# Kernel optimization log

Measured on AMD Instinct MI355X. Metric: run time of the kernel, lower is better.

Reference implementation:

```python
import jax, jax.numpy as jnp
import numpy as np

N_NODES = 50000
N_EDGES = 800000
IN_DIM = 256
OUT_DIM = 64
NEG_SLOPE = 0.01  # torch F.leaky_relu default


def setup_inputs() -> dict:
    key = jax.random.key(0)
    k1, k2, k3, k4, k5 = jax.random.split(key, 5)
    h = jax.random.normal(k1, (N_NODES, IN_DIM), dtype=jnp.float32)
    W = jax.random.normal(k2, (OUT_DIM, IN_DIM), dtype=jnp.float32) * 0.05
    a = jax.random.normal(k3, (1, 2 * OUT_DIM), dtype=jnp.float32) * 0.05
    src = jax.random.randint(k4, (N_EDGES,), 0, N_NODES)
    dst = jax.random.randint(k5, (N_EDGES,), 0, N_NODES)
    return {"h": h, "W": W, "a": a, "src": src, "dst": dst}


def reference(h, W, a, src, dst):
    # node projection: z = fc(h)               [N, D_out]
    z = jnp.einsum("ni,oi->no", h, W)
    # edge attention: e = leaky_relu(attn_fc(concat(z_src, z_dst)))
    # split a into left/right halves to avoid materializing the [E, 2D] concat
    a_l, a_r = a[0, :OUT_DIM], a[0, OUT_DIM:]
    el = z @ a_l  # [N]
    er = z @ a_r  # [N]
    e = jax.nn.leaky_relu(el[src] + er[dst], negative_slope=NEG_SLOPE)  # [E]
    # segment softmax over incoming edges of each destination node
    m = jax.ops.segment_max(e, dst, num_segments=N_NODES)  # [N], -inf for isolated
    ex = jnp.exp(e - m[dst])                               # [E]
    s = jax.ops.segment_sum(ex, dst, num_segments=N_NODES)  # [N]
    alpha = ex / s[dst]                                     # [E]
    # weighted-sum aggregation of source features
    h_out = jax.ops.segment_sum(alpha[:, None] * z[src], dst, num_segments=N_NODES)
    return h_out
```

## Files before the change

kernel.cpp:

```cpp
#include <hip/hip_runtime.h>

#define IN_DIM 256
#define OUT_DIM 64
#define NEG_SLOPE 0.01f
#define CHUNK 4096

typedef __attribute__((ext_vector_type(8))) short short8v;
typedef __attribute__((ext_vector_type(4))) float float4v;

__device__ __forceinline__ unsigned short f2bf(float f) {
    unsigned u = __float_as_uint(f);
    return (unsigned short)((u + 0x7FFFu + ((u >> 16) & 1u)) >> 16);
}
__device__ __forceinline__ float bf2f(unsigned short u) {
    return __uint_as_float((unsigned)u << 16);
}

__global__ void k_init(const float* __restrict__ W, unsigned short* __restrict__ Wb,
                       int* __restrict__ bc, int* __restrict__ cursor) {
    int i = blockIdx.x * blockDim.x + threadIdx.x;
    if (i < OUT_DIM * IN_DIM) Wb[i] = f2bf(W[i]);
    if (i < 256) { bc[i] = 0; cursor[i] = 0; }
}

__global__ __launch_bounds__(256, 3) void k1_mfma_count(
        const float* __restrict__ h, const unsigned short* __restrict__ Wb,
        const float* __restrict__ a, const int* __restrict__ dst,
        unsigned short* __restrict__ zb, float* __restrict__ el, float* __restrict__ er,
        int* __restrict__ bc, int M, int E) {
    __shared__ uint4 wlds[2048];
    __shared__ int hist[256];
    hist[threadIdx.x] = 0;

    #pragma unroll
    for (int k = 0; k < 8; ++k) {
        int c = threadIdx.x + k * 256;
        int row = c >> 5, col = c & 31;
        wlds[(row << 5) | (col ^ (row & 7))] = ((const uint4*)Wb)[c];
    }
    __syncthreads();

    const int lane = threadIdx.x & 63;
    const int wid  = (blockIdx.x * 256 + threadIdx.x) >> 6;
    const int r0 = wid * 16;

    if (r0 < M) {
        const int lrow = lane & 15;
        const int kgrp = lane >> 4;
        const int k0   = kgrp * 8;
        const int swz  = lrow & 7;

        const float* __restrict__ hrow = h + (size_t)(r0 + lrow) * IN_DIM;

        float4 hreg[16];
        #pragma unroll
        for (int s = 0; s < 8; ++s) {
            hreg[2 * s]     = *(const float4*)(hrow + s * 32 + k0);
            hreg[2 * s + 1] = *(const float4*)(hrow + s * 32 + k0 + 4);
        }

        float4v acc[4];
        #pragma unroll
        for (int n = 0; n < 4; ++n) acc[n] = (float4v){0.f, 0.f, 0.f, 0.f};

        #pragma unroll
        for (int s = 0; s < 8; ++s) {
            float4 ha = hreg[2 * s], hb = hreg[2 * s + 1];
            short8v afrag;
            afrag[0] = (short)f2bf(ha.x); afrag[1] = (short)f2bf(ha.y);
            afrag[2] = (short)f2bf(ha.z); afrag[3] = (short)f2bf(ha.w);
            afrag[4] = (short)f2bf(hb.x); afrag[5] = (short)f2bf(hb.y);
            afrag[6] = (short)f2bf(hb.z); afrag[7] = (short)f2bf(hb.w);
            #pragma unroll
            for (int n = 0; n < 4; ++n) {
                const int slot = ((n * 16 + lrow) << 5) | ((s * 4 + kgrp) ^ swz);
                short8v bfrag = *(const short8v*)&wlds[slot];
                acc[n] = __builtin_amdgcn_mfma_f32_16x16x32_bf16(afrag, bfrag, acc[n], 0, 0, 0);
            }
        }

        float al4[4], ar4[4];
        #pragma unroll
        for (int n = 0; n < 4; ++n) {
            al4[n] = a[n * 16 + lrow];
            ar4[n] = a[OUT_DIM + n * 16 + lrow];
        }
        #pragma unroll
        for (int j = 0; j < 4; ++j) {
            const int row = r0 + kgrp * 4 + j;
            float vl = 0.f, vr = 0.f;
            #pragma unroll
            for (int n = 0; n < 4; ++n) {
                float v = acc[n][j];
                zb[(size_t)row * OUT_DIM + n * 16 + lrow] = f2bf(v);
                vl += v * al4[n];
                vr += v * ar4[n];
            }
            #pragma unroll
            for (int m = 8; m >= 1; m >>= 1) {
                vl += __shfl_xor(vl, m, 64);
                vr += __shfl_xor(vr, m, 64);
            }
            if (lrow == 0) { el[row] = vl; er[row] = vr; }
        }
    }

    __syncthreads();
    const int stride = gridDim.x * 256;
    for (int i = blockIdx.x * 256 + threadIdx.x; i < E; i += stride)
        atomicAdd(&hist[dst[i] >> 8], 1);
    __syncthreads();
    if (hist[threadIdx.x]) atomicAdd(&bc[threadIdx.x], hist[threadIdx.x]);
}

__global__ __launch_bounds__(256) void kA_scatter(
        const int* __restrict__ src, const int* __restrict__ dst,
        const int* __restrict__ bc, int* __restrict__ cursor,
        unsigned* __restrict__ bucketbuf, int E, int nbuck) {
    __shared__ unsigned stag[CHUNK];
    __shared__ int bsc[256], cnt[256], lofs[256], lcur[256], tb[256];
    const int t = threadIdx.x;
    const int base = blockIdx.x * CHUNK;
    const int n = min(CHUNK, E - base);

    int bv = (t < nbuck) ? bc[t] : 0;
    bsc[t] = bv;
    cnt[t] = 0;
    __syncthreads();
    for (int off = 1; off < 256; off <<= 1) {
        int add = (t >= off) ? bsc[t - off] : 0;
        __syncthreads();
        bsc[t] += add;
        __syncthreads();
    }
    const int bstart_t = bsc[t] - bv;

    int es[16], ed[16];
    #pragma unroll
    for (int k = 0; k < 16; ++k) {
        int p = t + k * 256;
        if (p < n) {
            es[k] = src[base + p];
            ed[k] = dst[base + p];
            atomicAdd(&cnt[ed[k] >> 8], 1);
        }
    }
    __syncthreads();

    lofs[t] = cnt[t];
    __syncthreads();
    for (int off = 1; off < 256; off <<= 1) {
        int add = (t >= off) ? lofs[t - off] : 0;
        __syncthreads();
        lofs[t] += add;
        __syncthreads();
    }
    lofs[t] -= cnt[t];
    __syncthreads();

    {
        int c = cnt[t];
        int g = c ? atomicAdd(&cursor[t], c) : 0;
        tb[t] = bstart_t + g - lofs[t];
    }
    lcur[t] = lofs[t];
    __syncthreads();

    #pragma unroll
    for (int k = 0; k < 16; ++k) {
        int p = t + k * 256;
        if (p < n) {
            int b = ed[k] >> 8;
            int pos = atomicAdd(&lcur[b], 1);
            stag[pos] = ((unsigned)ed[k] << 16) | (unsigned)es[k];
        }
    }
    __syncthreads();

    #pragma unroll
    for (int k = 0; k < 16; ++k) {
        int p = t + k * 256;
        if (p < n) {
            unsigned v = stag[p];
            int b = v >> 24;
            bucketbuf[tb[b] + p] = v;
        }
    }
}

__global__ __launch_bounds__(256) void kB_build(
        const unsigned* __restrict__ bucketbuf, const int* __restrict__ bc,
        int* __restrict__ csr_src, int* __restrict__ ends, int N, int nbuck) {
    __shared__ int sc[256], lcnt[256], lofs[256], lcur[256];
    __shared__ int s_start;
    const int b = blockIdx.x, t = threadIdx.x;

    int bv = (t < nbuck) ? bc[t] : 0;
    sc[t] = bv;
    lcnt[t] = 0;
    __syncthreads();
    for (int off = 1; off < 256; off <<= 1) {
        int add = (t >= off) ? sc[t - off] : 0;
        __syncthreads();
        sc[t] += add;
        __syncthreads();
    }
    if (t == b) s_start = sc[t] - bv;
    __syncthreads();

    const int start = s_start;
    const int cnt = bc[b];
    const int node0 = b << 8;
    const int nloc = min(256, N - node0);

    for (int i = t; i < cnt; i += 256)
        atomicAdd(&lcnt[(bucketbuf[start + i] >> 16) & 255], 1);
    __syncthreads();

    lofs[t] = lcnt[t];
    __syncthreads();
    for (int off = 1; off < 256; off <<= 1) {
        int add = (t >= off) ? lofs[t - off] : 0;
        __syncthreads();
        lofs[t] += add;
        __syncthreads();
    }
    if (t < nloc) ends[node0 + t] = start + lofs[t];
    lcur[t] = lofs[t] - lcnt[t];
    __syncthreads();

    for (int i = t; i < cnt; i += 256) {
        unsigned v = bucketbuf[start + i];
        int node = (v >> 16) & 255;
        int pos = atomicAdd(&lcur[node], 1);
        csr_src[start + pos] = (int)(v & 0xFFFFu);
    }
}

__global__ __launch_bounds__(256) void k5_node(
        const int* __restrict__ csr_src, const int* __restrict__ ends,
        const float* __restrict__ el, const float* __restrict__ er,
        const unsigned short* __restrict__ zb, float* __restrict__ out, int N) {
    const int lane = threadIdx.x & 63;
    const int node = blockIdx.x * 4 + (threadIdx.x >> 6);
    if (node >= N) return;

    const int start = (node == 0) ? 0 : ends[node - 1];
    const int end   = ends[node];
    const int deg   = end - start;
    float acc = 0.0f;

    if (deg > 0 && deg <= 64) {
        const float er_i = er[node];
        int   s0 = 0;
        float m  = -3.4e38f;
        float e0 = 0.0f;
        if (lane < deg) {
            s0 = csr_src[start + lane];
            float x = el[s0] + er_i;
            e0 = fmaxf(x, NEG_SLOPE * x);
            m  = e0;
        }
        #pragma unroll
        for (int msk = 32; msk; msk >>= 1) m = fmaxf(m, __shfl_xor(m, msk, 64));
        float ex0 = (lane < deg) ? __expf(e0 - m) : 0.0f;
        float sum = ex0;
        #pragma unroll
        for (int msk = 32; msk; msk >>= 1) sum += __shfl_xor(sum, msk, 64);
        const float inv = 1.0f / sum;

        float aq[8];
        #pragma unroll
        for (int q = 0; q < 8; ++q) aq[q] = 0.f;
        int r = 0;
        for (; r + 8 <= deg; r += 8) {
            int ss[8]; float ww[8];
            #pragma unroll
            for (int q = 0; q < 8; ++q) {
                ss[q] = __shfl(s0,  r + q, 64);
                ww[q] = __shfl(ex0, r + q, 64);
            }
            #pragma unroll
            for (int q = 0; q < 8; ++q)
                aq[q] += ww[q] * bf2f(zb[(size_t)ss[q] * OUT_DIM + lane]);
        }
        for (; r < deg; ++r) {
            int   sa = __shfl(s0,  r, 64);
            float wa = __shfl(ex0, r, 64);
            aq[0] += wa * bf2f(zb[(size_t)sa * OUT_DIM + lane]);
        }
        acc = (((aq[0] + aq[1]) + (aq[2] + aq[3])) +
               ((aq[4] + aq[5]) + (aq[6] + aq[7]))) * inv;
    } else if (deg > 64) {
        const float er_i = er[node];
        float e0 = 0.0f, e1 = 0.0f;
        int   s0 = 0,    s1 = 0;
        float m = -3.4e38f;
        int t = 0;
        for (int j = start + lane; j < end; j += 64, ++t) {
            int s = csr_src[j];
            float x = el[s] + er_i;
            float e = fmaxf(x, NEG_SLOPE * x);
            if (t == 0) { e0 = e; s0 = s; }
            else if (t == 1) { e1 = e; s1 = s; }
            m = fmaxf(m, e);
        }
        #pragma unroll
        for (int msk = 32; msk; msk >>= 1) m = fmaxf(m, __shfl_xor(m, msk, 64));
        float sum = 0.0f;
        t = 0;
        for (int j = start + lane; j < end; j += 64, ++t) {
            float e;
            if (t == 0) e = e0;
            else if (t == 1) e = e1;
            else {
                int s = csr_src[j];
                float x = el[s] + er_i;
                e = fmaxf(x, NEG_SLOPE * x);
            }
            float ex = __expf(e - m);
            if (t == 0) e0 = ex; else if (t == 1) e1 = ex;
            sum += ex;
        }
        #pragma unroll
        for (int msk = 32; msk; msk >>= 1) sum += __shfl_xor(sum, msk, 64);
        const float inv = 1.0f / sum;

        for (int r = 0; r < deg; ++r) {
            int tt = r >> 6, owner = r & 63;
            int s; float ex;
            if (tt == 0)      { s = __shfl(s0, owner, 64); ex = __shfl(e0, owner, 64); }
            else if (tt == 1) { s = __shfl(s1, owner, 64); ex = __shfl(e1, owner, 64); }
            else {
                s = csr_src[start + r];
                float x = el[s] + er_i;
                float e = fmaxf(x, NEG_SLOPE * x);
                ex = __expf(e - m);
            }
            acc += ex * bf2f(zb[(size_t)s * OUT_DIM + lane]);
        }
        acc *= inv;
    }
    out[(size_t)node * OUT_DIM + lane] = acc;
}

extern "C" void kernel_launch(void* const* d_in, const int* in_sizes, int n_in,
                              void* d_out, int out_size, void* d_ws, size_t ws_size,
                              hipStream_t stream) {
    const float* h   = (const float*)d_in[0];
    const float* W   = (const float*)d_in[1];
    const float* a   = (const float*)d_in[2];
    const int*   src = (const int*)d_in[3];
    const int*   dst = (const int*)d_in[4];
    float* out = (float*)d_out;

    const int N = in_sizes[0] / IN_DIM;
    const int E = in_sizes[3];
    const int nbuck = (N + 255) >> 8;

    unsigned short* zb = (unsigned short*)d_ws;
    float* el   = (float*)(zb + (size_t)N * OUT_DIM);
    float* er   = el + N;
    int*   ends = (int*)(er + N);
    int*   csr_src = ends + N;
    unsigned* bucketbuf = (unsigned*)(csr_src + E);
    int*   bc     = (int*)(bucketbuf + E);
    int*   cursor = bc + 256;
    unsigned short* Wb = (unsigned short*)(cursor + 256);

    k_init<<<(OUT_DIM * IN_DIM + 255) / 256, 256, 0, stream>>>(W, Wb, bc, cursor);
    {
        const int waves = (N + 15) / 16;
        k1_mfma_count<<<(waves + 3) / 4, 256, 0, stream>>>(h, Wb, a, dst, zb, el, er,
                                                           bc, N, E);
    }
    kA_scatter<<<(E + CHUNK - 1) / CHUNK, 256, 0, stream>>>(src, dst, bc, cursor,
                                                            bucketbuf, E, nbuck);
    kB_build<<<nbuck, 256, 0, stream>>>(bucketbuf, bc, csr_src, ends, N, nbuck);
    k5_node<<<(N + 3) / 4, 256, 0, stream>>>(csr_src, ends, el, er, zb, out, N);
}
```

Measured before the change: 95.42 us.

## Split wavefront into half-waves gathering two edges each, and shrink bucket chunk

```diff
diff --git a/kernel.cpp b/kernel.cpp
--- a/kernel.cpp
+++ b/kernel.cpp
@@ -3,7 +3,8 @@
 #define IN_DIM 256
 #define OUT_DIM 64
 #define NEG_SLOPE 0.01f
-#define CHUNK 4096
+#define CHUNK 1024
+#define KPT (CHUNK / 256)
 
 typedef __attribute__((ext_vector_type(8))) short short8v;
 typedef __attribute__((ext_vector_type(4))) float float4v;
@@ -135,9 +136,9 @@
     }
     const int bstart_t = bsc[t] - bv;
 
-    int es[16], ed[16];
+    int es[KPT], ed[KPT];
     #pragma unroll
-    for (int k = 0; k < 16; ++k) {
+    for (int k = 0; k < KPT; ++k) {
         int p = t + k * 256;
         if (p < n) {
             es[k] = src[base + p];
@@ -167,7 +168,7 @@
     __syncthreads();
 
     #pragma unroll
-    for (int k = 0; k < 16; ++k) {
+    for (int k = 0; k < KPT; ++k) {
         int p = t + k * 256;
         if (p < n) {
             int b = ed[k] >> 8;
@@ -178,7 +179,7 @@
     __syncthreads();
 
     #pragma unroll
-    for (int k = 0; k < 16; ++k) {
+    for (int k = 0; k < KPT; ++k) {
         int p = t + k * 256;
         if (p < n) {
             unsigned v = stag[p];
@@ -248,7 +249,10 @@
     const int start = (node == 0) ? 0 : ends[node - 1];
     const int end   = ends[node];
     const int deg   = end - start;
-    float acc = 0.0f;
+    const int half  = lane >> 5;
+    const int lh    = lane & 31;
+
+    float rlo = 0.f, rhi = 0.f;
 
     if (deg > 0 && deg <= 64) {
         const float er_i = er[node];
@@ -269,28 +273,42 @@
         for (int msk = 32; msk; msk >>= 1) sum += __shfl_xor(sum, msk, 64);
         const float inv = 1.0f / sum;
 
-        float aq[8];
-        #pragma unroll
-        for (int q = 0; q < 8; ++q) aq[q] = 0.f;
-        int r = 0;
-        for (; r + 8 <= deg; r += 8) {
-            int ss[8]; float ww[8];
+        const int npairs = (deg + 1) >> 1;
+        float2 acc0 = {0.f, 0.f}, acc1 = {0.f, 0.f},
+               acc2 = {0.f, 0.f}, acc3 = {0.f, 0.f};
+        int p = 0;
+        for (; p + 4 <= npairs; p += 4) {
             #pragma unroll
-            for (int q = 0; q < 8; ++q) {
-                ss[q] = __shfl(s0,  r + q, 64);
-                ww[q] = __shfl(ex0, r + q, 64);
-            }
-            #pragma unroll
-            for (int q = 0; q < 8; ++q)
-                aq[q] += ww[q] * bf2f(zb[(size_t)ss[q] * OUT_DIM + lane]);
-        }
-        for (; r < deg; ++r) {
-            int   sa = __shfl(s0,  r, 64);
-            float wa = __shfl(ex0, r, 64);
-            aq[0] += wa * bf2f(zb[(size_t)sa * OUT_DIM + lane]);
-        }
-        acc = (((aq[0] + aq[1]) + (aq[2] + aq[3])) +
-               ((aq[4] + aq[5]) + (aq[6] + aq[7]))) * inv;
+            for (int q = 0; q < 4; ++q) {
+                int e  = 2 * (p + q) + half;
+                int cl = (e < deg) ? e : (deg - 1);
+                float wv = __shfl(ex0, cl, 64);
+                int   sv = __shfl(s0,  cl, 64);
+                if (e >= deg) wv = 0.0f;
+                unsigned u = *(const unsigned*)(zb + (size_t)sv * OUT_DIM + lh * 2);
+                float zl = bf2f((unsigned short)(u & 0xFFFFu));
+                float zh = bf2f((unsigned short)(u >> 16));
+                if (q == 0) { acc0.x += wv * zl; acc0.y += wv * zh; }
+                else if (q == 1) { acc1.x += wv * zl; acc1.y += wv * zh; }
+                else if (q == 2) { acc2.x += wv * zl; acc2.y += wv * zh; }
+                else { acc3.x += wv * zl; acc3.y += wv * zh; }
+            }
+        }
+        for (; p < npairs; ++p) {
+            int e  = 2 * p + half;
+            int cl = (e < deg) ? e : (deg - 1);
+            float wv = __shfl(ex0, cl, 64);
+            int   sv = __shfl(s0,  cl, 64);
+            if (e >= deg) wv = 0.0f;
+            unsigned u = *(const unsigned*)(zb + (size_t)sv * OUT_DIM + lh * 2);
+            acc0.x += wv * bf2f((unsigned short)(u & 0xFFFFu));
+            acc0.y += wv * bf2f((unsigned short)(u >> 16));
+        }
+        rlo = ((acc0.x + acc1.x) + (acc2.x + acc3.x));
+        rhi = ((acc0.y + acc1.y) + (acc2.y + acc3.y));
+        rlo += __shfl_xor(rlo, 32, 64);
+        rhi += __shfl_xor(rhi, 32, 64);
+        rlo *= inv; rhi *= inv;
     } else if (deg > 64) {
         const float er_i = er[node];
         float e0 = 0.0f, e1 = 0.0f;
@@ -326,6 +344,7 @@
         for (int msk = 32; msk; msk >>= 1) sum += __shfl_xor(sum, msk, 64);
         const float inv = 1.0f / sum;
 
+        float acc = 0.0f;
         for (int r = 0; r < deg; ++r) {
             int tt = r >> 6, owner = r & 63;
             int s; float ex;
@@ -340,8 +359,14 @@
             acc += ex * bf2f(zb[(size_t)s * OUT_DIM + lane]);
         }
         acc *= inv;
-    }
-    out[(size_t)node * OUT_DIM + lane] = acc;
+        rlo = __shfl(acc, 2 * lh, 64);
+        rhi = __shfl(acc, 2 * lh + 1, 64);
+    }
+
+    if (lane < 32) {
+        float2 o; o.x = rlo; o.y = rhi;
+        *(float2*)(out + (size_t)node * OUT_DIM + lh * 2) = o;
+    }
 }
 
 extern "C" void kernel_launch(void* const* d_in, const int* in_sizes, int n_in,
```

New measurement: 97.13 us. Within noise of the previous version (+1.8%).
